# Kernel optimization log

Measured on AMD Instinct MI355X. Metric: run time of the kernel, lower is better.

Reference implementation:

```python
import jax, jax.numpy as jnp
import numpy as np

D_MODEL = 1024
NHEAD = 16
HEAD_DIM = D_MODEL // NHEAD


def setup_inputs() -> dict:
    key = jax.random.key(0)
    ks = jax.random.split(key, 11)
    B, S = 2, 2048
    scale = 1.0 / np.sqrt(D_MODEL)
    inp = {
        "query": jax.random.normal(ks[0], (B, S, D_MODEL), jnp.float32),
        "key": jax.random.normal(ks[1], (B, S, D_MODEL), jnp.float32),
        "value": jax.random.normal(ks[2], (B, S, D_MODEL), jnp.float32),
        "Wq": jax.random.normal(ks[3], (D_MODEL, D_MODEL), jnp.float32) * scale,
        "bq": jnp.zeros((D_MODEL,), jnp.float32),
        "Wk": jax.random.normal(ks[4], (D_MODEL, D_MODEL), jnp.float32) * scale,
        "bk": jnp.zeros((D_MODEL,), jnp.float32),
        "Wv": jax.random.normal(ks[5], (D_MODEL, D_MODEL), jnp.float32) * scale,
        "bv": jnp.zeros((D_MODEL,), jnp.float32),
        "Wo": jax.random.normal(ks[6], (D_MODEL, D_MODEL), jnp.float32) * scale,
        "bo": jnp.zeros((D_MODEL,), jnp.float32),
    }
    return inp


def reference(query, key, value, Wq, bq, Wk, bk, Wv, bv, Wo, bo):
    B, S, _ = query.shape
    # Linear projections (torch Linear: x @ W.T + b)
    def proj(x, W, b):
        y = x @ W.T + b
        return y.reshape(B, -1, NHEAD, HEAD_DIM).transpose(0, 2, 1, 3)  # [B,H,S,hd]
    q = proj(query, Wq, bq)
    k = proj(key, Wk, bk)
    v = proj(value, Wv, bv)
    scores = jnp.einsum("bhqd,bhkd->bhqk", q, k) / np.sqrt(HEAD_DIM)
    attn = jax.nn.softmax(scores, axis=-1)  # dropout is identity (eval / p=0)
    out = jnp.einsum("bhqk,bhkd->bhqd", attn, v)
    out = out.transpose(0, 2, 1, 3).reshape(B, S, D_MODEL)
    return out @ Wo.T + bo
```

## Files before the change

kernel.cpp:

```cpp
#include <hip/hip_runtime.h>
#include <stdint.h>

typedef __attribute__((ext_vector_type(8))) short bf16x8;
typedef __attribute__((ext_vector_type(4))) short bf16x4;
typedef __attribute__((ext_vector_type(4))) float f32x4;
typedef __attribute__((ext_vector_type(16))) float f32x16;
typedef __attribute__((ext_vector_type(2))) unsigned int u32x2;
typedef __attribute__((ext_vector_type(4))) unsigned int u32x4;
typedef unsigned int u32;
typedef unsigned short u16;

#define S_LEN 2048
#define DMODEL 1024
#define HD 64


static __device__ __forceinline__ u16 f2bf(float f) {
  u32 u = __builtin_bit_cast(u32, f);
  return (u16)((u + 0x7fffu + ((u >> 16) & 1u)) >> 16);
}

static __device__ __forceinline__ u32 cvt_pk(float a, float b) {
  u32 r;
  asm("v_cvt_pk_bf16_f32 %0, %1, %2" : "=v"(r) : "v"(a), "v"(b));
  return r;
}

static __device__ __forceinline__ void gl_lds16(const u16* g, u16* l) {
  __builtin_amdgcn_global_load_lds((const __attribute__((address_space(1))) u32*)g,
                                   (__attribute__((address_space(3))) u32*)l, 16, 0, 0);
}

static __device__ __forceinline__ u32 lds_addr(const void* p) {
  return (u32)(uint64_t)p;
}

static __device__ __forceinline__ bf16x4 tr16(u32 addr) {
  bf16x4 r;
  asm volatile("ds_read_b64_tr_b16 %0, %1" : "=v"(r) : "v"(addr));
  return r;
}

__global__ __launch_bounds__(256) void convert_w(
    const float* __restrict__ wq, const float* __restrict__ wk,
    const float* __restrict__ wv, const float* __restrict__ wo,
    u16* __restrict__ dst) {
  size_t i = ((size_t)blockIdx.x * 256 + threadIdx.x) * 8;
  u32 wsel = (u32)((i >> 20) & 3u);
  const float* src = (wsel == 0) ? wq : (wsel == 1) ? wk : (wsel == 2) ? wv : wo;
  size_t off = i & 0xFFFFFu;
  float4 a = *(const float4*)(src + off);
  float4 b = *(const float4*)(src + off + 4);
  bf16x8 o;
  o[0] = (short)f2bf(a.x); o[1] = (short)f2bf(a.y);
  o[2] = (short)f2bf(a.z); o[3] = (short)f2bf(a.w);
  o[4] = (short)f2bf(b.x); o[5] = (short)f2bf(b.y);
  o[6] = (short)f2bf(b.z); o[7] = (short)f2bf(b.w);
  *(bf16x8*)(dst + i) = o;
}

template <int OUT_BF16, int BN>
static __device__ __forceinline__ void gemm_core(
    const u16* __restrict__ A, const u16* __restrict__ Bm,
    const float* __restrict__ bias, void* __restrict__ Y, float scale,
    int bm, int bn, u16* As, u16* Bs) {
  const int tid = threadIdx.x;
  const int lane = tid & 63, w = tid >> 6;
  const int wm = w >> 1, wn = w & 1;
  const int g = lane >> 4, l15 = lane & 15;
  constexpr int NFR = BN / 64 * 2;

  f32x4 acc[4][NFR] = {};

  const int r0 = tid >> 2, k8 = (tid & 3) * 8;
  const int r1 = (tid + 256) >> 2;
  const size_t arow0 = (size_t)(bm * 128 + r0) * DMODEL + k8;
  const size_t arow1 = (size_t)(bm * 128 + r1) * DMODEL + k8;
  const size_t brow0 = (size_t)(bn * BN + r0) * DMODEL + k8;
  const size_t brow1 = (size_t)(bn * BN + r1) * DMODEL + k8;

  auto stage = [&](int buf, int kt) {
    const int kb = kt * 32;
    u16* asb = As + buf * 4096;
    u16* bsb = Bs + buf * (BN * 32);
    gl_lds16(A + arow0 + kb, asb + w * 512);
    gl_lds16(A + arow1 + kb, asb + w * 512 + 2048);
    gl_lds16(Bm + brow0 + kb, bsb + w * 512);
    if constexpr (BN == 128) gl_lds16(Bm + brow1 + kb, bsb + w * 512 + 2048);
  };

  stage(0, 0);
  __syncthreads();
  int cur = 0;
  for (int kt = 0; kt < 32; ++kt) {
    if (kt < 31) stage(cur ^ 1, kt + 1);
    const u16* as = As + cur * 4096;
    const u16* bs = Bs + cur * (BN * 32);
    bf16x8 a[4], b[NFR];
#pragma unroll
    for (int mi = 0; mi < 4; ++mi)
      a[mi] = *(const bf16x8*)&as[(wm * 64 + mi * 16 + l15) * 32 + g * 8];
#pragma unroll
    for (int ni = 0; ni < NFR; ++ni)
      b[ni] = *(const bf16x8*)&bs[(wn * (BN / 2) + ni * 16 + l15) * 32 + g * 8];
#pragma unroll
    for (int mi = 0; mi < 4; ++mi)
#pragma unroll
      for (int ni = 0; ni < NFR; ++ni)
        acc[mi][ni] = __builtin_amdgcn_mfma_f32_16x16x32_bf16(a[mi], b[ni], acc[mi][ni], 0, 0, 0);
    __syncthreads();
    cur ^= 1;
  }

#pragma unroll
  for (int ni = 0; ni < NFR; ++ni) {
    const int col = bn * BN + wn * (BN / 2) + ni * 16 + l15;
    const float bv = bias[col];
#pragma unroll
    for (int mi = 0; mi < 4; ++mi) {
      const int row0 = bm * 128 + wm * 64 + mi * 16 + g * 4;
#pragma unroll
      for (int r = 0; r < 4; ++r) {
        float v = (acc[mi][ni][r] + bv) * scale;
        if (OUT_BF16)
          ((u16*)Y)[(size_t)(row0 + r) * DMODEL + col] = f2bf(v);
        else
          ((float*)Y)[(size_t)(row0 + r) * DMODEL + col] = v;
      }
    }
  }
}

__global__ __launch_bounds__(256) void qkv_gemm(
    const float* __restrict__ xq, const float* __restrict__ xk, const float* __restrict__ xv,
    const u16* __restrict__ W,
    const float* __restrict__ bq, const float* __restrict__ bk, const float* __restrict__ bv,
    u16* __restrict__ Qp, u16* __restrict__ Kpp, u16* __restrict__ Vpp, float qscale) {
  __shared__ u16 As[2 * 4096];
  __shared__ u16 Bs[2 * 4096];
  const int sel = blockIdx.x >> 8;
  const int bb = blockIdx.x & 255;
  const int bm = (bb & 7) * 4 + (bb >> 6);
  const int bn = (bb >> 3) & 7;
  const float* A = (sel == 0) ? xq : (sel == 1) ? xk : xv;
  const u16* Bm = W + (size_t)sel * (1024 * 1024);
  const float* bias = (sel == 0) ? bq : (sel == 1) ? bk : bv;
  u16* Y = (sel == 0) ? Qp : (sel == 1) ? Kpp : Vpp;
  const float scale = (sel == 0) ? qscale : 1.0f;

  const int tid = threadIdx.x;
  const int lane = tid & 63, w = tid >> 6;
  const int wm = w >> 1, wn = w & 1;
  const int g = lane >> 4, l15 = lane & 15;

  f32x4 acc[4][4] = {};

  const int r0 = tid >> 2, k8 = (tid & 3) * 8;
  const int r1 = (tid + 256) >> 2;
  const size_t arow0 = (size_t)(bm * 128 + r0) * DMODEL + k8;
  const size_t arow1 = (size_t)(bm * 128 + r1) * DMODEL + k8;
  const size_t brow0 = (size_t)(bn * 128 + r0) * DMODEL + k8;
  const size_t brow1 = (size_t)(bn * 128 + r1) * DMODEL + k8;

  float4 af0, af1, af2, af3;
  auto loadA = [&](int kt) {
    const int kb = kt * 32;
    af0 = *(const float4*)(A + arow0 + kb);
    af1 = *(const float4*)(A + arow0 + kb + 4);
    af2 = *(const float4*)(A + arow1 + kb);
    af3 = *(const float4*)(A + arow1 + kb + 4);
  };
  auto writeA = [&](int buf) {
    u16* asb = As + buf * 4096;
    u32x4 p0 = {cvt_pk(af0.x, af0.y), cvt_pk(af0.z, af0.w),
                cvt_pk(af1.x, af1.y), cvt_pk(af1.z, af1.w)};
    u32x4 p1 = {cvt_pk(af2.x, af2.y), cvt_pk(af2.z, af2.w),
                cvt_pk(af3.x, af3.y), cvt_pk(af3.z, af3.w)};
    *(u32x4*)(asb + tid * 8) = p0;
    *(u32x4*)(asb + tid * 8 + 2048) = p1;
  };
  auto stageB = [&](int buf, int kt) {
    const int kb = kt * 32;
    u16* bsb = Bs + buf * 4096;
    gl_lds16(Bm + brow0 + kb, bsb + w * 512);
    gl_lds16(Bm + brow1 + kb, bsb + w * 512 + 2048);
  };

  loadA(0);
  stageB(0, 0);
  writeA(0);
  __syncthreads();
  int cur = 0;
  for (int kt = 0; kt < 32; ++kt) {
    if (kt < 31) {
      loadA(kt + 1);
      stageB(cur ^ 1, kt + 1);
    }
    const u16* as = As + cur * 4096;
    const u16* bs = Bs + cur * 4096;
    bf16x8 a[4], b[4];
#pragma unroll
    for (int mi = 0; mi < 4; ++mi)
      a[mi] = *(const bf16x8*)&as[(wm * 64 + mi * 16 + l15) * 32 + g * 8];
#pragma unroll
    for (int ni = 0; ni < 4; ++ni)
      b[ni] = *(const bf16x8*)&bs[(wn * 64 + ni * 16 + l15) * 32 + g * 8];
#pragma unroll
    for (int mi = 0; mi < 4; ++mi)
#pragma unroll
      for (int ni = 0; ni < 4; ++ni)
        acc[mi][ni] = __builtin_amdgcn_mfma_f32_16x16x32_bf16(a[mi], b[ni], acc[mi][ni], 0, 0, 0);
    if (kt < 31) writeA(cur ^ 1);
    __syncthreads();
    cur ^= 1;
  }

#pragma unroll
  for (int ni = 0; ni < 4; ++ni) {
    const int col = bn * 128 + wn * 64 + ni * 16 + l15;
    const float bv = bias[col];
#pragma unroll
    for (int mi = 0; mi < 4; ++mi) {
      const int row0 = bm * 128 + wm * 64 + mi * 16 + g * 4;
#pragma unroll
      for (int r = 0; r < 4; ++r) {
        float v = (acc[mi][ni][r] + bv) * scale;
        ((u16*)Y)[(size_t)(row0 + r) * DMODEL + col] = f2bf(v);
      }
    }
  }
}

__global__ __launch_bounds__(256) void wo_gemm(
    const u16* __restrict__ A, const u16* __restrict__ Bm,
    const float* __restrict__ bias, float* __restrict__ Y) {
  __shared__ u16 As[2 * 4096];
  __shared__ u16 Bs[2 * 2048];
  const int idx = blockIdx.x;
  const int bm = (idx & 7) * 4 + (idx >> 7);
  const int bn = (idx >> 3) & 15;
  gemm_core<0, 64>(A, Bm, bias, Y, 1.0f, bm, bn, As, Bs);
}

__global__ __launch_bounds__(512, 4) void attn_fwd(
    const u16* __restrict__ Qp, const u16* __restrict__ Kp,
    const u16* __restrict__ Vp, u16* __restrict__ Op) {
  __shared__ u16 smem[16384];
  const int tid = threadIdx.x;
  const int lane = tid & 63, w = tid >> 6;
  const int hi = lane >> 5, l31 = lane & 31;
  const int qs = w & 3, hf = w >> 2;
  const int bh = blockIdx.x >> 4;
  const int qt = blockIdx.x & 15;
  const int b = bh >> 4, h = bh & 15;
  const size_t rowbase = (size_t)b * S_LEN;
  const int hcol = h * HD;

  bf16x8 qf[4];
  {
    const size_t qoff = (rowbase + qt * 128 + qs * 32 + l31) * DMODEL + hcol + hi * 8;
#pragma unroll
    for (int dblk = 0; dblk < 4; ++dblk)
      qf[dblk] = *(const bf16x8*)(Qp + qoff + dblk * 16);
  }

  f32x16 o0 = {}, o1 = {};
  float lsum = 0.0f;

  const u32 sbase = lds_addr(smem);

  const int half_s = tid >> 8;
  const int kvs = (tid >> 3) & 31, slot = (tid & 7) ^ (kvs & 7);
  const size_t koff = (rowbase + half_s * 1024 + kvs) * (size_t)DMODEL + hcol + slot * 8;
  const int cv = tid & 255;
  const int cc2 = cv & 1, jj = (cv >> 1) & 3, dh_s = (cv >> 3) & 1,
            kvg_s = (cv >> 4) & 7, db_s = (cv >> 7) & 1;
  const size_t voff = (rowbase + half_s * 1024 + kvg_s * 4 + jj) * (size_t)DMODEL
                      + hcol + db_s * 32 + dh_s * 16 + cc2 * 8;

  auto stage = [&](int buf, int it) {
    const size_t adv = (size_t)it * 32 * DMODEL;
    gl_lds16(Kp + koff + adv, smem + buf * 8192 + w * 512);
    gl_lds16(Vp + voff + adv, smem + buf * 8192 + 4096 + w * 512);
  };

  stage(0, 0);
  __syncthreads();
  int cur = 0;
  const int dh = (lane >> 4) & 1, c15 = lane & 15;
  for (int it = 0; it < 32; ++it) {
    if (it < 31) stage(cur ^ 1, it + 1);
    const char* kb = (const char*)smem + cur * 16384 + hf * 4096;
    const u32 vb = sbase + (u32)(cur * 16384 + 8192 + hf * 4096);

    f32x16 sA = {};
    __builtin_amdgcn_s_setprio(1);
#pragma unroll
    for (int dblk = 0; dblk < 4; ++dblk) {
      const u32 sl = (u32)((dblk * 2 + hi) ^ (l31 & 7));
      bf16x8 kf = *(const bf16x8*)(kb + l31 * 128 + sl * 16);
      sA = __builtin_amdgcn_mfma_f32_32x32x16_bf16(kf, qf[dblk], sA, 0, 0, 0);
    }
    __builtin_amdgcn_s_setprio(0);

    u32 w0[4], w1[4];
    float psum = 0.0f;
#pragma unroll
    for (int bq = 0; bq < 4; ++bq) {
      float e0 = __builtin_amdgcn_exp2f(sA[4 * bq + 0]);
      float e1 = __builtin_amdgcn_exp2f(sA[4 * bq + 1]);
      float e2 = __builtin_amdgcn_exp2f(sA[4 * bq + 2]);
      float e3 = __builtin_amdgcn_exp2f(sA[4 * bq + 3]);
      psum += (e0 + e1) + (e2 + e3);
      w0[bq] = cvt_pk(e0, e1);
      w1[bq] = cvt_pk(e2, e3);
    }
    psum += __shfl_xor(psum, 32);
    lsum += psum;

    bf16x8 pa[2];
#pragma unroll
    for (int kblk = 0; kblk < 2; ++kblk) {
      u32 xa = w0[2 * kblk], ya = w0[2 * kblk + 1];
      asm("v_permlane32_swap_b32 %0, %1" : "+v"(xa), "+v"(ya));
      u32 xb = w1[2 * kblk], yb = w1[2 * kblk + 1];
      asm("v_permlane32_swap_b32 %0, %1" : "+v"(xb), "+v"(yb));
      u32x4 pw = {xa, xb, ya, yb};
      pa[kblk] = __builtin_bit_cast(bf16x8, pw);
    }

    bf16x4 tv[2][2][2];
#pragma unroll
    for (int dblk = 0; dblk < 2; ++dblk)
#pragma unroll
      for (int kblk = 0; kblk < 2; ++kblk)
#pragma unroll
        for (int r = 0; r < 2; ++r)
          tv[dblk][kblk][r] =
              tr16(vb + (u32)(dblk * 2048 + (4 * kblk + 2 * hi + r) * 256 + dh * 128 + c15 * 8));
    asm volatile("s_waitcnt lgkmcnt(0)" ::: "memory");
    __builtin_amdgcn_sched_barrier(0);
    __builtin_amdgcn_s_setprio(1);
#pragma unroll
    for (int kblk = 0; kblk < 2; ++kblk) {
      bf16x8 vf0, vf1;
#pragma unroll
      for (int j = 0; j < 4; ++j) {
        vf0[j] = tv[0][kblk][0][j]; vf0[4 + j] = tv[0][kblk][1][j];
        vf1[j] = tv[1][kblk][0][j]; vf1[4 + j] = tv[1][kblk][1][j];
      }
      o0 = __builtin_amdgcn_mfma_f32_32x32x16_bf16(pa[kblk], vf0, o0, 0, 0, 0);
      o1 = __builtin_amdgcn_mfma_f32_32x32x16_bf16(pa[kblk], vf1, o1, 0, 0, 0);
    }
    __builtin_amdgcn_s_setprio(0);
    __syncthreads();
    cur ^= 1;
  }

  float* smf = (float*)smem;
  if (w >= 4 && lane < 32) smf[(w - 4) * 32 + lane] = lsum;
  __syncthreads();
  float linv = 0.0f;
  if (w < 4) linv = 1.0f / (lsum + smf[w * 32 + l31]);
  __syncthreads();
  if (w >= 4) {
    char* ob = (char*)smem + (w - 4) * 8192;
#pragma unroll
    for (int q4 = 0; q4 < 4; ++q4) {
      f32x4 v0 = {o0[4 * q4 + 0], o0[4 * q4 + 1], o0[4 * q4 + 2], o0[4 * q4 + 3]};
      f32x4 v1 = {o1[4 * q4 + 0], o1[4 * q4 + 1], o1[4 * q4 + 2], o1[4 * q4 + 3]};
      *(f32x4*)(ob + q4 * 1024 + lane * 16) = v0;
      *(f32x4*)(ob + (4 + q4) * 1024 + lane * 16) = v1;
    }
  }
  __syncthreads();
  if (w < 4) {
    const char* ob = (const char*)smem + w * 8192;
    float li[16];
#pragma unroll
    for (int r = 0; r < 16; ++r) {
      const int qr = (r & 3) + 8 * (r >> 2) + 4 * hi;
      li[r] = __shfl(linv, qr);
    }
#pragma unroll
    for (int q4 = 0; q4 < 4; ++q4) {
      f32x4 p0 = *(const f32x4*)(ob + q4 * 1024 + lane * 16);
      f32x4 p1 = *(const f32x4*)(ob + (4 + q4) * 1024 + lane * 16);
#pragma unroll
      for (int j = 0; j < 4; ++j) {
        const int r = 4 * q4 + j;
        const int qr = (r & 3) + 8 * (r >> 2) + 4 * hi;
        const size_t orow = (rowbase + qt * 128 + qs * 32 + qr) * DMODEL + hcol;
        Op[orow + l31] = f2bf((o0[r] + p0[j]) * li[r]);
        Op[orow + 32 + l31] = f2bf((o1[r] + p1[j]) * li[r]);
      }
    }
  }
}

extern "C" void kernel_launch(void* const* d_in, const int* in_sizes, int n_in,
                              void* d_out, int out_size, void* d_ws, size_t ws_size,
                              hipStream_t stream) {
  const float* xq = (const float*)d_in[0];
  const float* xk = (const float*)d_in[1];
  const float* xv = (const float*)d_in[2];
  const float* Wq = (const float*)d_in[3];
  const float* bq = (const float*)d_in[4];
  const float* Wk = (const float*)d_in[5];
  const float* bk = (const float*)d_in[6];
  const float* Wv = (const float*)d_in[7];
  const float* bv = (const float*)d_in[8];
  const float* Wo = (const float*)d_in[9];
  const float* bo = (const float*)d_in[10];

  u16* ws = (u16*)d_ws;
  const size_t MB4 = 4096ull * 1024ull;
  u16* WQb = ws + 3 * MB4;
  u16* Qp = ws + 4 * MB4;
  u16* Kpp = ws + 5 * MB4;
  u16* Vpp = ws + 6 * MB4;
  u16* Opp = ws + 7 * MB4;

  convert_w<<<2048, 256, 0, stream>>>(Wq, Wk, Wv, Wo, WQb);

  const float qscale = 0.125f * 1.44269504088896340736f;
  qkv_gemm<<<768, 256, 0, stream>>>(xq, xk, xv, WQb, bq, bk, bv, Qp, Kpp, Vpp, qscale);

  attn_fwd<<<512, 512, 0, stream>>>(Qp, Kpp, Vpp, Opp);

  wo_gemm<<<512, 256, 0, stream>>>(Opp, WQb + 3 * 1024 * 1024, bo, (float*)d_out);
}
```

Measured before the change: 117.8 us.

## Prefetch A tiles two iterations ahead and remap attention blocks per XCD

The QKV projection GEMM now keeps two register buffers for the fp32 A tile and issues global loads two k-steps ahead, giving the loads more time to arrive before they are converted to bf16 and written to LDS. The attention kernel remaps block indices so that all query tiles of the same batch-head land on the same XCD, aiming to improve L2 reuse of K/V. The deeper prefetch costs extra VGPRs, which may lower occupancy. Selecting the buffer through a runtime ternary on a register array could also force the array into scratch memory.

```diff
diff --git a/kernel.cpp b/kernel.cpp
--- a/kernel.cpp
+++ b/kernel.cpp
@@ -162,20 +162,20 @@
   const size_t brow0 = (size_t)(bn * 128 + r0) * DMODEL + k8;
   const size_t brow1 = (size_t)(bn * 128 + r1) * DMODEL + k8;
 
-  float4 af0, af1, af2, af3;
-  auto loadA = [&](int kt) {
+  float4 afA[4], afB[4];
+  auto loadA = [&](int kt, float4* dst) {
     const int kb = kt * 32;
-    af0 = *(const float4*)(A + arow0 + kb);
-    af1 = *(const float4*)(A + arow0 + kb + 4);
-    af2 = *(const float4*)(A + arow1 + kb);
-    af3 = *(const float4*)(A + arow1 + kb + 4);
+    dst[0] = *(const float4*)(A + arow0 + kb);
+    dst[1] = *(const float4*)(A + arow0 + kb + 4);
+    dst[2] = *(const float4*)(A + arow1 + kb);
+    dst[3] = *(const float4*)(A + arow1 + kb + 4);
   };
-  auto writeA = [&](int buf) {
+  auto writeA = [&](int buf, const float4* src) {
     u16* asb = As + buf * 4096;
-    u32x4 p0 = {cvt_pk(af0.x, af0.y), cvt_pk(af0.z, af0.w),
-                cvt_pk(af1.x, af1.y), cvt_pk(af1.z, af1.w)};
-    u32x4 p1 = {cvt_pk(af2.x, af2.y), cvt_pk(af2.z, af2.w),
-                cvt_pk(af3.x, af3.y), cvt_pk(af3.z, af3.w)};
+    u32x4 p0 = {cvt_pk(src[0].x, src[0].y), cvt_pk(src[0].z, src[0].w),
+                cvt_pk(src[1].x, src[1].y), cvt_pk(src[1].z, src[1].w)};
+    u32x4 p1 = {cvt_pk(src[2].x, src[2].y), cvt_pk(src[2].z, src[2].w),
+                cvt_pk(src[3].x, src[3].y), cvt_pk(src[3].z, src[3].w)};
     *(u32x4*)(asb + tid * 8) = p0;
     *(u32x4*)(asb + tid * 8 + 2048) = p1;
   };
@@ -186,16 +186,15 @@
     gl_lds16(Bm + brow1 + kb, bsb + w * 512 + 2048);
   };
 
-  loadA(0);
+  loadA(0, afA);
   stageB(0, 0);
-  writeA(0);
+  loadA(1, afB);
+  writeA(0, afA);
   __syncthreads();
   int cur = 0;
   for (int kt = 0; kt < 32; ++kt) {
-    if (kt < 31) {
-      loadA(kt + 1);
-      stageB(cur ^ 1, kt + 1);
-    }
+    if (kt < 31) stageB(cur ^ 1, kt + 1);
+    if (kt < 30) loadA(kt + 2, (kt & 1) ? afB : afA);
     const u16* as = As + cur * 4096;
     const u16* bs = Bs + cur * 4096;
     bf16x8 a[4], b[4];
@@ -210,7 +209,7 @@
 #pragma unroll
       for (int ni = 0; ni < 4; ++ni)
         acc[mi][ni] = __builtin_amdgcn_mfma_f32_16x16x32_bf16(a[mi], b[ni], acc[mi][ni], 0, 0, 0);
-    if (kt < 31) writeA(cur ^ 1);
+    if (kt < 31) writeA(cur ^ 1, ((kt + 1) & 1) ? afB : afA);
     __syncthreads();
     cur ^= 1;
   }
@@ -250,8 +249,10 @@
   const int lane = tid & 63, w = tid >> 6;
   const int hi = lane >> 5, l31 = lane & 31;
   const int qs = w & 3, hf = w >> 2;
-  const int bh = blockIdx.x >> 4;
-  const int qt = blockIdx.x & 15;
+  const int xcd = blockIdx.x & 7;
+  const int idx = blockIdx.x >> 3;
+  const int bh = xcd * 4 + (idx >> 4);
+  const int qt = idx & 15;
   const int b = bh >> 4, h = bh & 15;
   const size_t rowbase = (size_t)b * S_LEN;
   const int hcol = h * HD;
```

Result: slower. 242.8 us (+106.0%).
